# Kernel optimization log

Hardware: AMD Instinct MI355X
Metric: run time of the kernel (lower is better)

The kernel has to match this reference:

```python
import jax, jax.numpy as jnp
import numpy as np

B, T, D = 2, 2048, 1024
N, K, H = 16, 8, 128  # q heads, kv heads, head_dim
G = N // K            # GQA group size
EPS = 1e-6
THETA = 1000000.0
SCALE = H ** -0.5
K_MASK = float(np.finfo(np.float32).min)


def rms_norm(x, scale):
    # RMSNorm over head_dim (last axis), computed in fp32 like the original
    dtype = x.dtype
    rms = jnp.sqrt(jnp.mean(x.astype(jnp.float32) ** 2, axis=-1, keepdims=True) + EPS)
    return (scale * x / rms).astype(dtype)


def positions_from_segment_ids(seg):
    t = jnp.arange(seg.shape[1], dtype=jnp.int32)[None, :]
    off = jnp.argmax(seg, axis=1, keepdims=True).astype(jnp.int32)
    rel = t - off
    return jnp.where(seg != 0, rel, jnp.int32(2 ** 30))


def rope_sin_cos(positions):
    frac = jnp.arange(0, H, 2, dtype=jnp.float32) / H
    inv_freq = 1.0 / (THETA ** frac)                    # [H/2]
    ang = positions.astype(jnp.float32)[..., None] * inv_freq  # [B,T,H/2]
    return jnp.sin(ang), jnp.cos(ang)


def apply_rope(x, sin, cos):
    # x: [B,T,heads,H]; sin/cos: [B,T,H/2]
    x1, x2 = x[..., : H // 2], x[..., H // 2:]
    s, c = sin[:, :, None, :], cos[:, :, None, :]
    return jnp.concatenate([x1 * c - x2 * s, x2 * c + x1 * s], axis=-1).astype(x.dtype)


def setup_inputs() -> dict:
    key = jax.random.key(0)
    ks = jax.random.split(key, 8)
    std = 0.02
    return {
        "x": jax.random.normal(ks[0], (B, T, D), dtype=jnp.float32),
        "segment_ids": jnp.ones((B, T), dtype=jnp.int32),
        "wq": jax.random.normal(ks[1], (D, N, H), dtype=jnp.float32) * std,
        "wk": jax.random.normal(ks[2], (D, K, H), dtype=jnp.float32) * std,
        "wv": jax.random.normal(ks[3], (D, K, H), dtype=jnp.float32) * std,
        "wo": jax.random.normal(ks[4], (N, H, D), dtype=jnp.float32) * std,
        "q_scale": jnp.ones((H,), dtype=jnp.float32),
        "k_scale": jnp.ones((H,), dtype=jnp.float32),
    }


def reference(x, segment_ids, wq, wk, wv, wo, q_scale, k_scale):
    # QKV projections + QK RMSNorm
    q = rms_norm(jnp.einsum('BTD,DNH->BTNH', x, wq), q_scale)  # [B,T,N,H]
    k = rms_norm(jnp.einsum('BSD,DKH->BSKH', x, wk), k_scale)  # [B,T,K,H]
    v = jnp.einsum('BSD,DKH->BSKH', x, wv)                     # [B,T,K,H]

    # RoPE using segment-relative positions
    pos = positions_from_segment_ids(segment_ids)  # [B,T] int32
    sin, cos = rope_sin_cos(pos)
    q = apply_rope(q, sin, cos)
    k = apply_rope(k, sin, cos)

    # GQA attention: [B,T,K,G,H] x [B,S,K,H] -> [B,T,S,K,G]
    qg = q.reshape(B, T, K, G, H)
    logits = jnp.einsum('BTKGH,BSKH->BTSKG', qg, k) * SCALE

    causal = pos[:, None, :] <= pos[:, :, None]                       # [B,T,S]
    segm = segment_ids[:, None, :] == segment_ids[:, :, None]         # [B,T,S]
    mask = (causal & segm)[:, :, :, None, None]
    logits = jnp.where(mask, logits, K_MASK)

    w = jax.nn.softmax(logits.astype(jnp.float32), axis=2).astype(logits.dtype)
    out = jnp.einsum('BTSKG,BSKH->BTKGH', w, v).reshape(B, T, N, H)
    return jnp.einsum('BTNH,NHD->BTD', out, wo)
```

## Files before the change

### kernel.cpp

```cpp
#include <hip/hip_runtime.h>
#include <hip/hip_bf16.h>


typedef unsigned short u16;
typedef __attribute__((ext_vector_type(8))) short s16x8;
typedef __attribute__((ext_vector_type(4))) float fp32x4;
typedef __attribute__((ext_vector_type(4))) u16 u16x4;

#define MFMA_BF16(a, b, c) __builtin_amdgcn_mfma_f32_16x16x32_bf16((a), (b), (c), 0, 0, 0)

static constexpr int Bq = 2, Tq = 2048, Dq = 1024, NHq = 16, KHq = 8, Hq = 128;
static constexpr float EPSq = 1e-6f;
static constexpr float S2q = 0.08838834764831845f * 1.4426950408889634f;
static constexpr float MAXq = 20.0f;
static constexpr float NEGHUGE = -3.0e38f;

__device__ __forceinline__ u16 f2b(float f) {
  __hip_bfloat16 h = __float2bfloat16(f);
  return *reinterpret_cast<u16*>(&h);
}

__device__ __forceinline__ void gload16(const u16* g, u16* lds_base) {
  __builtin_amdgcn_global_load_lds(
      (const __attribute__((address_space(1))) unsigned int*)(const void*)g,
      (__attribute__((address_space(3))) unsigned int*)(void*)lds_base, 16, 0, 0);
}


__global__ __launch_bounds__(256) void prep_kernel(
    const float* __restrict__ x, const float* __restrict__ wq,
    const float* __restrict__ wk, const float* __restrict__ wv,
    const float* __restrict__ wo, const int* __restrict__ seg,
    u16* __restrict__ xb, u16* __restrict__ wqkv_t, u16* __restrict__ wo_t,
    int* __restrict__ pos) {
  const int bid = blockIdx.x;
  const int tid = threadIdx.x;
  if (bid < 4096) {
    const int i = bid * 1024 + tid * 4;
    const float4 v = *reinterpret_cast<const float4*>(x + i);
    u16x4 o;
    o.x = f2b(v.x); o.y = f2b(v.y); o.z = f2b(v.z); o.w = f2b(v.w);
    *reinterpret_cast<u16x4*>(xb + i) = o;
    return;
  }
  __shared__ float tile[32][33];
  __shared__ int sv[256], si[256];
  const int tx = tid & 31, ty = tid >> 5;
  if (bid < 8192) {
    const int z = bid - 4096;
    const int r0 = (z & 31) * 32;
    const int c0 = (z >> 5) * 32;
    const float* src;
    int stride, coff;
    if (c0 < 2048)      { src = wq; stride = 2048; coff = c0; }
    else if (c0 < 3072) { src = wk; stride = 1024; coff = c0 - 2048; }
    else                { src = wv; stride = 1024; coff = c0 - 3072; }
#pragma unroll
    for (int j = 0; j < 32; j += 8)
      tile[ty + j][tx] = src[(long)(r0 + ty + j) * stride + (coff + tx)];
    __syncthreads();
#pragma unroll
    for (int j = 0; j < 32; j += 8)
      wqkv_t[(long)(c0 + ty + j) * 1024 + (r0 + tx)] = f2b(tile[tx][ty + j]);
    return;
  }
  if (bid < 10240) {
    const int z = bid - 8192;
    const int c0 = (z & 31) * 32;
    const int r0 = (z >> 5) * 32;
#pragma unroll
    for (int j = 0; j < 32; j += 8)
      tile[ty + j][tx] = wo[(long)(r0 + ty + j) * 1024 + (c0 + tx)];
    __syncthreads();
#pragma unroll
    for (int j = 0; j < 32; j += 8)
      wo_t[(long)(c0 + ty + j) * 2048 + (r0 + tx)] = f2b(tile[tx][ty + j]);
    return;
  }
  const int b = bid - 10240;
  const int* s = seg + b * Tq;
  int bestv = -2147483647 - 1, besti = 0x7fffffff;
  for (int t = tid; t < Tq; t += 256) {
    int v = s[t];
    if (v > bestv) { bestv = v; besti = t; }
  }
  sv[tid] = bestv; si[tid] = besti;
  __syncthreads();
  for (int k = 128; k > 0; k >>= 1) {
    if (tid < k) {
      int v2 = sv[tid + k], i2 = si[tid + k];
      if (v2 > sv[tid] || (v2 == sv[tid] && i2 < si[tid])) {
        sv[tid] = v2; si[tid] = i2;
      }
    }
    __syncthreads();
  }
  const int off = si[0];
  for (int t = tid; t < Tq; t += 256)
    pos[b * Tq + t] = (s[t] != 0) ? (t - off) : (1 << 30);
}


__global__ __launch_bounds__(256) void gemm_qkv_kernel(
    const u16* __restrict__ A, const u16* __restrict__ Bt,
    u16* __restrict__ qkv, u16* __restrict__ vt, const int* __restrict__ pos,
    const float* __restrict__ q_scale, const float* __restrict__ k_scale) {
  __shared__ __align__(16) u16 As[128][64];
  __shared__ __align__(16) u16 Bs[128][64];
  const int tid = threadIdx.x;
  const int wave = tid >> 6, lane = tid & 63;
  const int quad = lane >> 4, l16 = lane & 15;
  const int m0 = blockIdx.y * 128, n0 = blockIdx.x * 128;
  const int row8 = lane >> 3;
  const int cgl = (lane & 7) ^ row8;

  const fp32x4 z4 = {0.f, 0.f, 0.f, 0.f};
  fp32x4 acc[2][8];
#pragma unroll
  for (int i = 0; i < 2; ++i)
#pragma unroll
    for (int j = 0; j < 8; ++j) acc[i][j] = z4;

  for (int k0 = 0; k0 < 1024; k0 += 64) {
    __syncthreads();
#pragma unroll
    for (int jj = 0; jj < 4; ++jj) {
      const int R = wave * 32 + jj * 8;
      gload16(A + (size_t)(m0 + R + row8) * 1024 + k0 + cgl * 8, &As[R][0]);
      gload16(Bt + (size_t)(n0 + R + row8) * 1024 + k0 + cgl * 8, &Bs[R][0]);
    }
    __syncthreads();
#pragma unroll
    for (int kh = 0; kh < 2; ++kh) {
      s16x8 af[2], bfr[8];
#pragma unroll
      for (int i = 0; i < 2; ++i)
        af[i] = *(const s16x8*)&As[wave * 32 + i * 16 + l16]
                               [((((kh << 2) | quad) ^ (l16 & 7)) << 3)];
#pragma unroll
      for (int j = 0; j < 8; ++j)
        bfr[j] = *(const s16x8*)&Bs[j * 16 + l16]
                                [((((kh << 2) | quad) ^ (l16 & 7)) << 3)];
#pragma unroll
      for (int i = 0; i < 2; ++i)
#pragma unroll
        for (int j = 0; j < 8; ++j) acc[i][j] = MFMA_BF16(af[i], bfr[j], acc[i][j]);
    }
  }

  const int wrow = m0 + wave * 32;
  if (n0 >= 3072) {
    const int kv8 = (n0 - 3072) >> 7;
    const int bq = wrow >> 11;
    const size_t vbase = (size_t)(bq * KHq + kv8) * Hq * Tq;
#pragma unroll
    for (int i = 0; i < 2; ++i) {
      const int t = (wrow + i * 16 + quad * 4) & 2047;
#pragma unroll
      for (int j = 0; j < 8; ++j) {
        const int h = j * 16 + l16;
        u16x4 o;
#pragma unroll
        for (int r = 0; r < 4; ++r) o[r] = f2b(acc[i][j][r]);
        *reinterpret_cast<u16x4*>(&vt[vbase + (size_t)h * Tq + t]) = o;
      }
    }
    return;
  }
  const float* scp = (n0 < 2048) ? q_scale : k_scale;
  float scl[8];
#pragma unroll
  for (int j = 0; j < 8; ++j) scl[j] = scp[j * 16 + l16];
  float invf[4];
#pragma unroll
  for (int jf = 0; jf < 4; ++jf)
    invf[jf] = __builtin_amdgcn_exp2f(
                   -(float)(jf * 16 + l16) * (19.931568569324174f / 64.0f)) *
               0.15915494309189535f;
#pragma unroll
  for (int i = 0; i < 2; ++i) {
    float ss[4] = {0.f, 0.f, 0.f, 0.f};
#pragma unroll
    for (int j = 0; j < 8; ++j)
#pragma unroll
      for (int r = 0; r < 4; ++r) ss[r] += acc[i][j][r] * acc[i][j][r];
#pragma unroll
    for (int d = 1; d < 16; d <<= 1)
#pragma unroll
      for (int r = 0; r < 4; ++r) ss[r] += __shfl_xor(ss[r], d, 64);
#pragma unroll
    for (int r = 0; r < 4; ++r) {
      const int row = wrow + i * 16 + quad * 4 + r;
      const float rinv = rsqrtf(ss[r] * (1.0f / 128.0f) + EPSq);
      const float P = (float)pos[row];
      u16* orow = qkv + (size_t)row * 4096 + n0;
#pragma unroll
      for (int jf = 0; jf < 4; ++jf) {
        float rev = P * invf[jf];
        rev -= floorf(rev);
        const float s = __builtin_amdgcn_sinf(rev);
        const float c = __builtin_amdgcn_cosf(rev);
        const float a1 = acc[i][jf][r] * rinv * scl[jf];
        const float a2 = acc[i][jf + 4][r] * rinv * scl[jf + 4];
        orow[jf * 16 + l16] = f2b(a1 * c - a2 * s);
        orow[(jf + 4) * 16 + l16] = f2b(a2 * c + a1 * s);
      }
    }
  }
}


__global__ __launch_bounds__(256) void gemm_out_kernel(
    const u16* __restrict__ A, const u16* __restrict__ Bt,
    float* __restrict__ C) {
  __shared__ __align__(16) u16 As[128][64];
  __shared__ __align__(16) u16 Bs[64][64];
  const int tid = threadIdx.x;
  const int wave = tid >> 6, lane = tid & 63;
  const int quad = lane >> 4, l16 = lane & 15;
  const int m0 = blockIdx.y * 128, n0 = blockIdx.x * 64;
  const int wm = (wave >> 1) * 64, wn = (wave & 1) * 32;
  const int row8 = lane >> 3;
  const int cgl = (lane & 7) ^ row8;

  const fp32x4 z4 = {0.f, 0.f, 0.f, 0.f};
  fp32x4 acc[4][2];
#pragma unroll
  for (int i = 0; i < 4; ++i)
#pragma unroll
    for (int j = 0; j < 2; ++j) acc[i][j] = z4;

  for (int k0 = 0; k0 < 2048; k0 += 64) {
    __syncthreads();
#pragma unroll
    for (int jj = 0; jj < 4; ++jj) {
      const int R = wave * 32 + jj * 8;
      gload16(A + (size_t)(m0 + R + row8) * 2048 + k0 + cgl * 8, &As[R][0]);
    }
#pragma unroll
    for (int jj = 0; jj < 2; ++jj) {
      const int R = wave * 16 + jj * 8;
      gload16(Bt + (size_t)(n0 + R + row8) * 2048 + k0 + cgl * 8, &Bs[R][0]);
    }
    __syncthreads();
#pragma unroll
    for (int kh = 0; kh < 2; ++kh) {
      s16x8 af[4], bfr[2];
#pragma unroll
      for (int i = 0; i < 4; ++i)
        af[i] = *(const s16x8*)&As[wm + i * 16 + l16]
                               [((((kh << 2) | quad) ^ (l16 & 7)) << 3)];
#pragma unroll
      for (int j = 0; j < 2; ++j)
        bfr[j] = *(const s16x8*)&Bs[wn + j * 16 + l16]
                                [((((kh << 2) | quad) ^ (l16 & 7)) << 3)];
#pragma unroll
      for (int i = 0; i < 4; ++i)
#pragma unroll
        for (int j = 0; j < 2; ++j) acc[i][j] = MFMA_BF16(af[i], bfr[j], acc[i][j]);
    }
  }
#pragma unroll
  for (int i = 0; i < 4; ++i) {
    const int row = m0 + wm + i * 16 + quad * 4;
#pragma unroll
    for (int j = 0; j < 2; ++j) {
      const int col = n0 + wn + j * 16 + l16;
#pragma unroll
      for (int r = 0; r < 4; ++r)
        C[(size_t)(row + r) * 1024 + col] = acc[i][j][r];
    }
  }
}


__global__ __launch_bounds__(256, 2) void flash_kernel(
    const u16* __restrict__ qkv, const u16* __restrict__ vt,
    const int* __restrict__ pos, const int* __restrict__ seg,
    u16* __restrict__ Obuf) {
  const int tid = threadIdx.x;
  const int w = tid >> 6;
  const int lane = tid & 63;
  const int quad = lane >> 4, l16 = lane & 15;
  const int g = blockIdx.x;
  const int b = g & 1;
  const int kv = (g >> 1) & 7;
  const int qh = kv * 2 + ((g >> 4) & 1);
  const int p = g >> 5;

  __shared__ __align__(16) u16 Ks[64][128];
  __shared__ __align__(16) u16 Vs[128][64];
  __shared__ __align__(16) u16 Ps[4][16][72];

  const u16* kbase = qkv + (size_t)(b * Tq) * 4096 + 2048 + kv * Hq;
  const u16* vbase = vt + (size_t)(b * KHq + kv) * Hq * Tq;
  const int krow_off = lane >> 4;
  const int vrow_off = lane >> 3;
  const fp32x4 z4 = {0.f, 0.f, 0.f, 0.f};
  const short one_bf = (short)0x3F80;
  const s16x8 ones = {one_bf, one_bf, one_bf, one_bf,
                      one_bf, one_bf, one_bf, one_bf};

#pragma unroll
  for (int phase = 0; phase < 2; ++phase) {
    const int c = phase ? p : 31 - p;
    const int t0 = c * 64 + w * 16;
    const int nst = c + 1;

    s16x8 qf[4];
    {
      const u16* qrow = qkv + (size_t)(b * Tq + t0 + l16) * 4096 + qh * Hq;
#pragma unroll
      for (int ks = 0; ks < 4; ++ks)
        qf[ks] = *(const s16x8*)(qrow + ks * 32 + quad * 8);
    }
    int my_pos[4], my_seg[4];
#pragma unroll
    for (int i = 0; i < 4; ++i) {
      const int t = t0 + quad * 4 + i;
      my_pos[i] = pos[b * Tq + t];
      my_seg[i] = seg[b * Tq + t];
    }
    fp32x4 l_acc = z4;
    fp32x4 o_acc[8];
#pragma unroll
    for (int h = 0; h < 8; ++h) o_acc[h] = z4;

    for (int st = 0; st < nst; ++st) {
      const int s0 = st * 64;
      __syncthreads();
#pragma unroll
      for (int j = 0; j < 4; ++j) {
        const int R = w * 16 + j * 4;
        const int r = R + krow_off;
        const int cg = (lane & 15) ^ (r & 15);
        gload16(kbase + (size_t)(s0 + r) * 4096 + cg * 8, &Ks[R][0]);
      }
#pragma unroll
      for (int j = 0; j < 4; ++j) {
        const int R = w * 32 + j * 8;
        const int r = R + vrow_off;
        const int cg = (lane & 7) ^ (vrow_off & 7);
        gload16(vbase + (size_t)r * Tq + s0 + cg * 8, &Vs[R][0]);
      }
      __syncthreads();

      fp32x4 sc[4];
#pragma unroll
      for (int sub = 0; sub < 4; ++sub) sc[sub] = z4;
#pragma unroll
      for (int sub = 0; sub < 4; ++sub)
#pragma unroll
        for (int ks = 0; ks < 4; ++ks) {
          const s16x8 kf =
              *(const s16x8*)&Ks[sub * 16 + l16][((((ks << 2) | quad) ^ l16) << 3)];
          sc[sub] = MFMA_BF16(qf[ks], kf, sc[sub]);
        }

      if (st == nst - 1) {
        int spos[4], sseg[4];
#pragma unroll
        for (int sub = 0; sub < 4; ++sub) {
          const int s = s0 + sub * 16 + l16;
          spos[sub] = pos[b * Tq + s];
          sseg[sub] = seg[b * Tq + s];
        }
#pragma unroll
        for (int sub = 0; sub < 4; ++sub)
#pragma unroll
          for (int i = 0; i < 4; ++i) {
            const bool ok = (sseg[sub] == my_seg[i]) && (spos[sub] <= my_pos[i]);
            sc[sub][i] = ok ? sc[sub][i] * S2q - MAXq : NEGHUGE;
          }
      } else {
#pragma unroll
        for (int sub = 0; sub < 4; ++sub)
#pragma unroll
          for (int i = 0; i < 4; ++i) sc[sub][i] = sc[sub][i] * S2q - MAXq;
      }

#pragma unroll
      for (int sub = 0; sub < 4; ++sub)
#pragma unroll
        for (int i = 0; i < 4; ++i)
          Ps[w][quad * 4 + i][sub * 16 + l16] =
              f2b(__builtin_amdgcn_exp2f(sc[sub][i]));
      asm volatile("s_waitcnt lgkmcnt(0)" ::: "memory");
      s16x8 pf[2];
#pragma unroll
      for (int kk = 0; kk < 2; ++kk)
        pf[kk] = *(const s16x8*)&Ps[w][l16][kk * 32 + quad * 8];

      l_acc = MFMA_BF16(pf[0], ones, l_acc);
      l_acc = MFMA_BF16(pf[1], ones, l_acc);
#pragma unroll
      for (int j = 0; j < 8; ++j)
#pragma unroll
        for (int kk = 0; kk < 2; ++kk) {
          const s16x8 vf =
              *(const s16x8*)&Vs[j * 16 + l16]
                             [((((kk << 2) | quad) ^ (l16 & 7)) << 3)];
          o_acc[j] = MFMA_BF16(pf[kk], vf, o_acc[j]);
        }
    }

    float inv[4];
#pragma unroll
    for (int i = 0; i < 4; ++i)
      inv[i] = (l_acc[i] > 0.f) ? 1.f / l_acc[i] : 0.f;
#pragma unroll
    for (int j = 0; j < 8; ++j)
#pragma unroll
      for (int i = 0; i < 4; ++i) {
        const int t = t0 + quad * 4 + i;
        Obuf[(size_t)(b * Tq + t) * 2048 + qh * Hq + j * 16 + l16] =
            f2b(o_acc[j][i] * inv[i]);
      }
  }
}


extern "C" void kernel_launch(void* const* d_in, const int* in_sizes, int n_in,
                              void* d_out, int out_size, void* d_ws, size_t ws_size,
                              hipStream_t stream) {
  const float* x = (const float*)d_in[0];
  const int* seg = (const int*)d_in[1];
  const float* wq = (const float*)d_in[2];
  const float* wk = (const float*)d_in[3];
  const float* wv = (const float*)d_in[4];
  const float* wo = (const float*)d_in[5];
  const float* q_scale = (const float*)d_in[6];
  const float* k_scale = (const float*)d_in[7];
  float* out = (float*)d_out;

  char* ws = (char*)d_ws;
  u16* xb = (u16*)(ws);
  u16* wqkv_t = (u16*)(ws + 8388608);
  u16* qkv = (u16*)(ws + 16777216);
  u16* vt = (u16*)(ws + 50331648);
  u16* wo_t = (u16*)(ws + 58720256);
  u16* Obuf = (u16*)(ws + 62914560);
  int* posb = (int*)(ws + 79691776);

  prep_kernel<<<10242, 256, 0, stream>>>(x, wq, wk, wv, wo, seg,
                                         xb, wqkv_t, wo_t, posb);

  gemm_qkv_kernel<<<dim3(32, 32, 1), 256, 0, stream>>>(
      xb, wqkv_t, qkv, vt, posb, q_scale, k_scale);

  flash_kernel<<<512, 256, 0, stream>>>(qkv, vt, posb, seg, Obuf);

  gemm_out_kernel<<<dim3(16, 32, 1), 256, 0, stream>>>(Obuf, wo_t, out);
}
```

Baseline: 231.8 us.

## Use 32x32 MFMA tiles in flash attention and deepen out-projection K tile

The flash kernel moves from 16x16x32 to 32x32x16 bf16 MFMAs and splits the four waves 2x2 over query rows and key/head columns. The probability tile is shared through LDS between the two waves that own a row block, which needs an extra block-wide barrier per key tile. The aim is fewer LDS fragment reads per MFMA and better matrix-core utilisation. Separately, the output-projection GEMM loads a 128-wide K slice per iteration with a 16-way XOR swizzle, halving the number of loop iterations and barriers at the cost of more LDS.

```diff
diff --git a/kernel.cpp b/kernel.cpp
--- a/kernel.cpp
+++ b/kernel.cpp
@@ -5,9 +5,11 @@
 typedef unsigned short u16;
 typedef __attribute__((ext_vector_type(8))) short s16x8;
 typedef __attribute__((ext_vector_type(4))) float fp32x4;
+typedef __attribute__((ext_vector_type(16))) float fp32x16;
 typedef __attribute__((ext_vector_type(4))) u16 u16x4;
 
 #define MFMA_BF16(a, b, c) __builtin_amdgcn_mfma_f32_16x16x32_bf16((a), (b), (c), 0, 0, 0)
+#define MFMA32(a, b, c) __builtin_amdgcn_mfma_f32_32x32x16_bf16((a), (b), (c), 0, 0, 0)
 
 static constexpr int Bq = 2, Tq = 2048, Dq = 1024, NHq = 16, KHq = 8, Hq = 128;
 static constexpr float EPSq = 1e-6f;
@@ -213,15 +215,15 @@
 __global__ __launch_bounds__(256) void gemm_out_kernel(
     const u16* __restrict__ A, const u16* __restrict__ Bt,
     float* __restrict__ C) {
-  __shared__ __align__(16) u16 As[128][64];
-  __shared__ __align__(16) u16 Bs[64][64];
+  __shared__ __align__(16) u16 As[128][128];
+  __shared__ __align__(16) u16 Bs[64][128];
   const int tid = threadIdx.x;
   const int wave = tid >> 6, lane = tid & 63;
   const int quad = lane >> 4, l16 = lane & 15;
   const int m0 = blockIdx.y * 128, n0 = blockIdx.x * 64;
   const int wm = (wave >> 1) * 64, wn = (wave & 1) * 32;
-  const int row8 = lane >> 3;
-  const int cgl = (lane & 7) ^ row8;
+  const int row4 = lane >> 4;
+  const int cgl16 = lane & 15;
 
   const fp32x4 z4 = {0.f, 0.f, 0.f, 0.f};
   fp32x4 acc[4][2];
@@ -230,30 +232,36 @@
 #pragma unroll
     for (int j = 0; j < 2; ++j) acc[i][j] = z4;
 
-  for (int k0 = 0; k0 < 2048; k0 += 64) {
-    __syncthreads();
+  for (int k0 = 0; k0 < 2048; k0 += 128) {
+    __syncthreads();
+#pragma unroll
+    for (int jj = 0; jj < 8; ++jj) {
+      const int R = wave * 32 + jj * 4;
+      const int r = R + row4;
+      const int cg = cgl16 ^ (r & 15);
+      gload16(A + (size_t)(m0 + r) * 2048 + k0 + cg * 8, &As[R][0]);
+    }
 #pragma unroll
     for (int jj = 0; jj < 4; ++jj) {
-      const int R = wave * 32 + jj * 8;
-      gload16(A + (size_t)(m0 + R + row8) * 2048 + k0 + cgl * 8, &As[R][0]);
-    }
-#pragma unroll
-    for (int jj = 0; jj < 2; ++jj) {
-      const int R = wave * 16 + jj * 8;
-      gload16(Bt + (size_t)(n0 + R + row8) * 2048 + k0 + cgl * 8, &Bs[R][0]);
-    }
-    __syncthreads();
-#pragma unroll
-    for (int kh = 0; kh < 2; ++kh) {
+      const int R = wave * 16 + jj * 4;
+      const int r = R + row4;
+      const int cg = cgl16 ^ (r & 15);
+      gload16(Bt + (size_t)(n0 + r) * 2048 + k0 + cg * 8, &Bs[R][0]);
+    }
+    __syncthreads();
+#pragma unroll
+    for (int kh = 0; kh < 4; ++kh) {
       s16x8 af[4], bfr[2];
 #pragma unroll
-      for (int i = 0; i < 4; ++i)
-        af[i] = *(const s16x8*)&As[wm + i * 16 + l16]
-                               [((((kh << 2) | quad) ^ (l16 & 7)) << 3)];
-#pragma unroll
-      for (int j = 0; j < 2; ++j)
-        bfr[j] = *(const s16x8*)&Bs[wn + j * 16 + l16]
-                                [((((kh << 2) | quad) ^ (l16 & 7)) << 3)];
+      for (int i = 0; i < 4; ++i) {
+        const int r = wm + i * 16 + l16;
+        af[i] = *(const s16x8*)&As[r][((((kh << 2) | quad) ^ (r & 15)) << 3)];
+      }
+#pragma unroll
+      for (int j = 0; j < 2; ++j) {
+        const int r = wn + j * 16 + l16;
+        bfr[j] = *(const s16x8*)&Bs[r][((((kh << 2) | quad) ^ (r & 15)) << 3)];
+      }
 #pragma unroll
       for (int i = 0; i < 4; ++i)
 #pragma unroll
@@ -281,7 +289,10 @@
   const int tid = threadIdx.x;
   const int w = tid >> 6;
   const int lane = tid & 63;
-  const int quad = lane >> 4, l16 = lane & 15;
+  const int l32 = lane & 31;
+  const int lh = lane >> 5;
+  const int rh = w & 1;
+  const int sh = w >> 1;
   const int g = blockIdx.x;
   const int b = g & 1;
   const int kv = (g >> 1) & 7;
@@ -290,13 +301,12 @@
 
   __shared__ __align__(16) u16 Ks[64][128];
   __shared__ __align__(16) u16 Vs[128][64];
-  __shared__ __align__(16) u16 Ps[4][16][72];
+  __shared__ __align__(16) u16 Ps[2][32][76];
 
   const u16* kbase = qkv + (size_t)(b * Tq) * 4096 + 2048 + kv * Hq;
   const u16* vbase = vt + (size_t)(b * KHq + kv) * Hq * Tq;
   const int krow_off = lane >> 4;
   const int vrow_off = lane >> 3;
-  const fp32x4 z4 = {0.f, 0.f, 0.f, 0.f};
   const short one_bf = (short)0x3F80;
   const s16x8 ones = {one_bf, one_bf, one_bf, one_bf,
                       one_bf, one_bf, one_bf, one_bf};
@@ -304,27 +314,25 @@
 #pragma unroll
   for (int phase = 0; phase < 2; ++phase) {
     const int c = phase ? p : 31 - p;
-    const int t0 = c * 64 + w * 16;
+    const int t0 = c * 64 + rh * 32;
     const int nst = c + 1;
 
-    s16x8 qf[4];
+    s16x8 qf[8];
     {
-      const u16* qrow = qkv + (size_t)(b * Tq + t0 + l16) * 4096 + qh * Hq;
-#pragma unroll
-      for (int ks = 0; ks < 4; ++ks)
-        qf[ks] = *(const s16x8*)(qrow + ks * 32 + quad * 8);
-    }
-    int my_pos[4], my_seg[4];
-#pragma unroll
-    for (int i = 0; i < 4; ++i) {
-      const int t = t0 + quad * 4 + i;
-      my_pos[i] = pos[b * Tq + t];
-      my_seg[i] = seg[b * Tq + t];
-    }
-    fp32x4 l_acc = z4;
-    fp32x4 o_acc[8];
-#pragma unroll
-    for (int h = 0; h < 8; ++h) o_acc[h] = z4;
+      const u16* qrow = qkv + (size_t)(b * Tq + t0 + l32) * 4096 + qh * Hq;
+#pragma unroll
+      for (int ks = 0; ks < 8; ++ks)
+        qf[ks] = *(const s16x8*)(qrow + ks * 16 + lh * 8);
+    }
+    int myp[16], mys[16];
+#pragma unroll
+    for (int r = 0; r < 16; ++r) {
+      const int t = t0 + 4 * lh + (r & 3) + 8 * (r >> 2);
+      myp[r] = pos[b * Tq + t];
+      mys[r] = seg[b * Tq + t];
+    }
+    fp32x16 l_acc = {};
+    fp32x16 o_acc[2] = {};
 
     for (int st = 0; st < nst; ++st) {
       const int s0 = st * 64;
@@ -345,76 +353,63 @@
       }
       __syncthreads();
 
-      fp32x4 sc[4];
-#pragma unroll
-      for (int sub = 0; sub < 4; ++sub) sc[sub] = z4;
-#pragma unroll
-      for (int sub = 0; sub < 4; ++sub)
+      fp32x16 sc = {};
+      const int srow = sh * 32 + l32;
+#pragma unroll
+      for (int ks = 0; ks < 8; ++ks) {
+        const s16x8 kf =
+            *(const s16x8*)&Ks[srow][((((ks << 1) | lh) ^ (l32 & 15)) << 3)];
+        sc = MFMA32(qf[ks], kf, sc);
+      }
+
+      const int scol = s0 + sh * 32 + l32;
+      const int spos = pos[b * Tq + scol];
+      const int sseg = seg[b * Tq + scol];
+      if (st == nst - 1) {
+#pragma unroll
+        for (int r = 0; r < 16; ++r) {
+          const bool ok = (sseg == mys[r]) && (spos <= myp[r]);
+          sc[r] = ok ? sc[r] * S2q - MAXq : NEGHUGE;
+        }
+      } else {
+#pragma unroll
+        for (int r = 0; r < 16; ++r) sc[r] = sc[r] * S2q - MAXq;
+      }
+#pragma unroll
+      for (int r = 0; r < 16; ++r)
+        Ps[rh][4 * lh + (r & 3) + 8 * (r >> 2)][sh * 32 + l32] =
+            f2b(__builtin_amdgcn_exp2f(sc[r]));
+      __syncthreads();
+
+      s16x8 pf[4];
+#pragma unroll
+      for (int ks = 0; ks < 4; ++ks)
+        pf[ks] = *(const s16x8*)&Ps[rh][l32][ks * 16 + lh * 8];
+#pragma unroll
+      for (int ks = 0; ks < 4; ++ks) l_acc = MFMA32(pf[ks], ones, l_acc);
+#pragma unroll
+      for (int nt = 0; nt < 2; ++nt) {
+        const int vrow = sh * 64 + nt * 32 + l32;
 #pragma unroll
         for (int ks = 0; ks < 4; ++ks) {
-          const s16x8 kf =
-              *(const s16x8*)&Ks[sub * 16 + l16][((((ks << 2) | quad) ^ l16) << 3)];
-          sc[sub] = MFMA_BF16(qf[ks], kf, sc[sub]);
+          const s16x8 vf =
+              *(const s16x8*)&Vs[vrow][((((ks << 1) | lh) ^ (l32 & 7)) << 3)];
+          o_acc[nt] = MFMA32(pf[ks], vf, o_acc[nt]);
         }
-
-      if (st == nst - 1) {
-        int spos[4], sseg[4];
-#pragma unroll
-        for (int sub = 0; sub < 4; ++sub) {
-          const int s = s0 + sub * 16 + l16;
-          spos[sub] = pos[b * Tq + s];
-          sseg[sub] = seg[b * Tq + s];
-        }
-#pragma unroll
-        for (int sub = 0; sub < 4; ++sub)
-#pragma unroll
-          for (int i = 0; i < 4; ++i) {
-            const bool ok = (sseg[sub] == my_seg[i]) && (spos[sub] <= my_pos[i]);
-            sc[sub][i] = ok ? sc[sub][i] * S2q - MAXq : NEGHUGE;
-          }
-      } else {
-#pragma unroll
-        for (int sub = 0; sub < 4; ++sub)
-#pragma unroll
-          for (int i = 0; i < 4; ++i) sc[sub][i] = sc[sub][i] * S2q - MAXq;
-      }
-
-#pragma unroll
-      for (int sub = 0; sub < 4; ++sub)
-#pragma unroll
-        for (int i = 0; i < 4; ++i)
-          Ps[w][quad * 4 + i][sub * 16 + l16] =
-              f2b(__builtin_amdgcn_exp2f(sc[sub][i]));
-      asm volatile("s_waitcnt lgkmcnt(0)" ::: "memory");
-      s16x8 pf[2];
-#pragma unroll
-      for (int kk = 0; kk < 2; ++kk)
-        pf[kk] = *(const s16x8*)&Ps[w][l16][kk * 32 + quad * 8];
-
-      l_acc = MFMA_BF16(pf[0], ones, l_acc);
-      l_acc = MFMA_BF16(pf[1], ones, l_acc);
-#pragma unroll
-      for (int j = 0; j < 8; ++j)
-#pragma unroll
-        for (int kk = 0; kk < 2; ++kk) {
-          const s16x8 vf =
-              *(const s16x8*)&Vs[j * 16 + l16]
-                             [((((kk << 2) | quad) ^ (l16 & 7)) << 3)];
-          o_acc[j] = MFMA_BF16(pf[kk], vf, o_acc[j]);
-        }
-    }
-
-    float inv[4];
-#pragma unroll
-    for (int i = 0; i < 4; ++i)
-      inv[i] = (l_acc[i] > 0.f) ? 1.f / l_acc[i] : 0.f;
-#pragma unroll
-    for (int j = 0; j < 8; ++j)
-#pragma unroll
-      for (int i = 0; i < 4; ++i) {
-        const int t = t0 + quad * 4 + i;
-        Obuf[(size_t)(b * Tq + t) * 2048 + qh * Hq + j * 16 + l16] =
-            f2b(o_acc[j][i] * inv[i]);
+      }
+    }
+
+    fp32x16 inv;
+#pragma unroll
+    for (int r = 0; r < 16; ++r)
+      inv[r] = (l_acc[r] > 0.f) ? 1.f / l_acc[r] : 0.f;
+#pragma unroll
+    for (int nt = 0; nt < 2; ++nt)
+#pragma unroll
+      for (int r = 0; r < 16; ++r) {
+        const int t = t0 + 4 * lh + (r & 3) + 8 * (r >> 2);
+        Obuf[(size_t)(b * Tq + t) * 2048 + qh * Hq + sh * 64 + nt * 32 + l32] =
+            f2b(o_acc[nt][r] * inv[r]);
       }
   }
 }
```

Result: no change. 235.5 us (+1.6%).
